# Kernel tuning notes

Hardware: AMD Instinct MI355X
Metric: run time of the kernel (lower is better)

Reference implementation:

```python
import jax, jax.numpy as jnp
import numpy as np

N = 100000   # nodes
E = 1600000  # edges
S = 4        # state_dimension
H = 64       # hidden_channels


def _gcn_conv(x, row, col, W, b):
    """PyG GCNConv: h = x @ W; add self-loops; symmetric deg^-1/2 norm; scatter-add; + bias."""
    n = x.shape[0]
    h = x @ W  # [N, out]
    loop = jnp.arange(n, dtype=row.dtype)
    r = jnp.concatenate([row, loop])  # sources (with self-loops)
    c = jnp.concatenate([col, loop])  # targets (with self-loops)
    deg = jax.ops.segment_sum(jnp.ones(r.shape[0], h.dtype), c, num_segments=n)
    dinv = jnp.where(deg > 0, jax.lax.rsqrt(deg), 0.0)
    norm = dinv[r] * dinv[c]                      # [E+N]
    msg = h[r] * norm[:, None]                    # gather + scale, [E+N, out]
    out = jax.ops.segment_sum(msg, c, num_segments=n)  # scatter-add
    return out + b


def setup_inputs() -> dict:
    key = jax.random.key(0)
    k1, k2, k3, k4 = jax.random.split(key, 4)
    x = jax.random.normal(k1, (N, S), dtype=jnp.float32)
    edge_index = jax.random.randint(k2, (2, E), 0, N, dtype=jnp.int32)
    # Glorot-ish init for the two GCNConv linear layers (+ zero bias, PyG default)
    W1 = jax.random.normal(k3, (S, H), dtype=jnp.float32) * (1.0 / np.sqrt(S))
    b1 = jnp.zeros((H,), jnp.float32)
    W2 = jax.random.normal(k4, (H, S), dtype=jnp.float32) * (1.0 / np.sqrt(H))
    b2 = jnp.zeros((S,), jnp.float32)
    return {"x": x, "edge_index": edge_index, "W1": W1, "b1": b1, "W2": W2, "b2": b2}


def reference(x, edge_index, W1, b1, W2, b2):
    row, col = edge_index[0], edge_index[1]
    h = _gcn_conv(x, row, col, W1, b1)
    h = jax.nn.relu(h)
    out = _gcn_conv(h, row, col, W2, b2)
    return out
```

## Files before the change

kernel.cpp:

```cpp
#include <hip/hip_runtime.h>


#define CSHIFT 10
#define CNODES 1024
#define KC_MAX 128
#define CAPC   18432
#define EPB    4096
#define CURPAD 16
#define HCAP   9216
#define ANODES 128
#define ACAP   2432

__global__ void k_zero(int* __restrict__ p, int n) {
    int i = blockIdx.x * blockDim.x + threadIdx.x;
    if (i < n) p[i] = 0;
}

__global__ void __launch_bounds__(512) k_part(
        const int* __restrict__ row, const int* __restrict__ col,
        int e, int Kc, int* __restrict__ cursor, unsigned* __restrict__ ere) {
    __shared__ int h[KC_MAX];
    __shared__ int loff[KC_MAX];
    __shared__ int gbase[KC_MAX];
    __shared__ int lcur[KC_MAX];
    __shared__ unsigned staged[EPB];
    int t = threadIdx.x;
    if (t < KC_MAX) h[t] = 0;
    __syncthreads();
    int lo = blockIdx.x * EPB;
    int cbuf[8], rbuf[8];
#pragma unroll
    for (int k = 0; k < 8; ++k) {
        int i = lo + t + k * 512;
        if (i < e) { cbuf[k] = col[i]; rbuf[k] = row[i]; }
        else { cbuf[k] = -1; rbuf[k] = 0; }
    }
#pragma unroll
    for (int k = 0; k < 8; ++k)
        if (cbuf[k] >= 0) atomicAdd(&h[cbuf[k] >> CSHIFT], 1);
    __syncthreads();
    if (t < KC_MAX) loff[t] = h[t];
    __syncthreads();
    for (int off = 1; off < KC_MAX; off <<= 1) {
        int v = (t < KC_MAX && t >= off) ? loff[t - off] : 0;
        __syncthreads();
        if (t < KC_MAX) loff[t] += v;
        __syncthreads();
    }
    if (t < KC_MAX) {
        int st = loff[t] - h[t];
        loff[t] = st;
        lcur[t] = st;
        if (t < Kc && h[t]) gbase[t] = atomicAdd(&cursor[t * CURPAD], h[t]);
    }
    __syncthreads();
#pragma unroll
    for (int k = 0; k < 8; ++k) {
        int c = cbuf[k];
        if (c < 0) continue;
        int pos = atomicAdd(&lcur[c >> CSHIFT], 1);
        staged[pos] = ((unsigned)rbuf[k] << CSHIFT) | (unsigned)(c & (CNODES - 1));
    }
    __syncthreads();
    int wid = t >> 6, lane = t & 63;
    for (int k = wid; k < Kc; k += 8) {
        int len = h[k];
        if (!len) continue;
        int gb = gbase[k], lb = loff[k];
        size_t dst = (size_t)k * CAPC + gb;
        for (int j = lane; j < len; j += 64)
            if (gb + j < CAPC) ere[dst + j] = staged[lb + j];
    }
}

__global__ void __launch_bounds__(1024) k_sortH(
        const int* __restrict__ cursor, unsigned* __restrict__ ere,
        int* __restrict__ rstart, const float4* __restrict__ x,
        float* __restrict__ dinv, float4* __restrict__ y, int n) {
    __shared__ int hist[CNODES];
    __shared__ int scn[CNODES];
    __shared__ unsigned sorted[HCAP];
    int b = blockIdx.x >> 1, half = blockIdx.x & 1;
    int t = threadIdx.x, nlo = b << CSHIFT;
    hist[t] = 0;
    __syncthreads();
    size_t c0 = (size_t)b * CAPC;
    int m = min(cursor[b * CURPAD], CAPC);
    int n4 = m >> 2;
    const uint4* e4 = (const uint4*)(ere + c0);
    for (int g = t; g < n4; g += 1024) {
        uint4 w = e4[g];
        atomicAdd(&hist[w.x & (CNODES - 1)], 1);
        atomicAdd(&hist[w.y & (CNODES - 1)], 1);
        atomicAdd(&hist[w.z & (CNODES - 1)], 1);
        atomicAdd(&hist[w.w & (CNODES - 1)], 1);
    }
    for (int i = (n4 << 2) + t; i < m; i += 1024)
        atomicAdd(&hist[ere[c0 + i] & (CNODES - 1)], 1);
    __syncthreads();
    int hv = hist[t];
    scn[t] = hv;
    __syncthreads();
    for (int off = 1; off < CNODES; off <<= 1) {
        int v = (t >= off) ? scn[t - off] : 0;
        __syncthreads();
        scn[t] += v;
        __syncthreads();
    }
    int st = scn[t] - hv;
    int hb1 = scn[511];
    rstart[(b << CSHIFT) + t] = (int)c0 + st;
    if ((t >> 9) == half) {
        int node = nlo + t;
        if (node < n) {
            float di = rsqrtf((float)hv + 1.0f);
            dinv[node] = di;
            float4 xv = x[node];
            y[node] = make_float4(xv.x * di, xv.y * di, xv.z * di, xv.w * di);
        }
    }
    int base = half ? hb1 : 0;
    int cnt = half ? (m - hb1) : hb1;
    __syncthreads();
    scn[t] = st - base;
    __syncthreads();
    for (int g = t; g < n4; g += 1024) {
        uint4 w = e4[g];
        int l0 = w.x & (CNODES - 1);
        if ((l0 >> 9) == half) { int p = atomicAdd(&scn[l0], 1); if (p < HCAP) sorted[p] = w.x >> CSHIFT; }
        int l1 = w.y & (CNODES - 1);
        if ((l1 >> 9) == half) { int p = atomicAdd(&scn[l1], 1); if (p < HCAP) sorted[p] = w.y >> CSHIFT; }
        int l2 = w.z & (CNODES - 1);
        if ((l2 >> 9) == half) { int p = atomicAdd(&scn[l2], 1); if (p < HCAP) sorted[p] = w.z >> CSHIFT; }
        int l3 = w.w & (CNODES - 1);
        if ((l3 >> 9) == half) { int p = atomicAdd(&scn[l3], 1); if (p < HCAP) sorted[p] = w.w >> CSHIFT; }
    }
    for (int i = (n4 << 2) + t; i < m; i += 1024) {
        unsigned w = ere[c0 + i];
        int ln = w & (CNODES - 1);
        if ((ln >> 9) == half) { int p = atomicAdd(&scn[ln], 1); if (p < HCAP) sorted[p] = w >> CSHIFT; }
    }
    __syncthreads();
    int wb = min(cnt, HCAP);
    for (int i = t; i < wb; i += 1024) ere[c0 + base + i] = sorted[i];
}

__global__ void __launch_bounds__(512) k_mid(
        const unsigned* __restrict__ ere, const int* __restrict__ rstart,
        const int* __restrict__ cursor, const float* __restrict__ dinv,
        const float4* __restrict__ x, const float4* __restrict__ y,
        const float* __restrict__ W1, const float* __restrict__ b1,
        const float* __restrict__ W2, const float* __restrict__ b2,
        float4* __restrict__ z, float4* __restrict__ out, int n) {
    __shared__ unsigned recs[ACAP];
    __shared__ float4 sums[ANODES];
    int g = blockIdx.x, t = threadIdx.x;
    int nlo = g * ANODES;
    int b = nlo >> CSHIFT;
    int c0i = (int)((size_t)b * CAPC);
    int s0 = rstart[nlo];
    int e0 = ((g & 7) == 7) ? c0i + min(cursor[b * CURPAD], CAPC)
                            : rstart[nlo + ANODES];
    int len = min(e0 - s0, ACAP);
    for (int i = t; i < len; i += 512) recs[i] = ere[s0 + i];
    __syncthreads();
    int tt = t >> 2, q = t & 3;
    int s = rstart[nlo + tt] - s0;
    int epos = (tt == ANODES - 1) ? len : min(rstart[nlo + tt + 1] - s0, len);
    float vx = 0.f, vy = 0.f, vz = 0.f, vw = 0.f;
    int i = s + q;
    while (i + 12 < epos) {
        int r0 = recs[i], r1 = recs[i + 4], r2 = recs[i + 8], r3 = recs[i + 12];
        float4 a0 = y[r0], a1 = y[r1], a2 = y[r2], a3 = y[r3];
        vx += a0.x + a1.x + a2.x + a3.x;
        vy += a0.y + a1.y + a2.y + a3.y;
        vz += a0.z + a1.z + a2.z + a3.z;
        vw += a0.w + a1.w + a2.w + a3.w;
        i += 16;
    }
    for (; i < epos; i += 4) {
        float4 a = y[recs[i]];
        vx += a.x; vy += a.y; vz += a.z; vw += a.w;
    }
    vx += __shfl_xor(vx, 1); vx += __shfl_xor(vx, 2);
    vy += __shfl_xor(vy, 1); vy += __shfl_xor(vy, 2);
    vz += __shfl_xor(vz, 1); vz += __shfl_xor(vz, 2);
    vw += __shfl_xor(vw, 1); vw += __shfl_xor(vw, 2);
    if (q == 0) sums[tt] = make_float4(vx, vy, vz, vw);
    __syncthreads();
    int node = nlo + t;
    if (t < ANODES && node < n) {
        float di = dinv[node], sl = di * di;
        float4 sv = sums[t];
        float4 xv = x[node];
        float a0 = di * sv.x + xv.x * sl;
        float a1 = di * sv.y + xv.y * sl;
        float a2 = di * sv.z + xv.z * sl;
        float a3 = di * sv.w + xv.w * sl;
        float t0 = 0.f, t1 = 0.f, t2 = 0.f, t3 = 0.f;
#pragma unroll 8
        for (int j = 0; j < 64; ++j) {
            float h = b1[j] + a0 * W1[j] + a1 * W1[64 + j] + a2 * W1[128 + j] + a3 * W1[192 + j];
            h = fmaxf(h, 0.f);
            t0 += h * W2[j * 4 + 0];
            t1 += h * W2[j * 4 + 1];
            t2 += h * W2[j * 4 + 2];
            t3 += h * W2[j * 4 + 3];
        }
        z[node] = make_float4(t0 * di, t1 * di, t2 * di, t3 * di);
        out[node] = make_float4(b2[0] + t0 * sl, b2[1] + t1 * sl,
                                b2[2] + t2 * sl, b2[3] + t3 * sl);
    }
}

__global__ void __launch_bounds__(512) k_acc2(
        const unsigned* __restrict__ ere, const int* __restrict__ rstart,
        const int* __restrict__ cursor, const float* __restrict__ dinv,
        const float4* __restrict__ z, float4* __restrict__ out, int n) {
    __shared__ unsigned recs[ACAP];
    __shared__ float4 sums[ANODES];
    int g = blockIdx.x, t = threadIdx.x;
    int nlo = g * ANODES;
    int b = nlo >> CSHIFT;
    int c0i = (int)((size_t)b * CAPC);
    int s0 = rstart[nlo];
    int e0 = ((g & 7) == 7) ? c0i + min(cursor[b * CURPAD], CAPC)
                            : rstart[nlo + ANODES];
    int len = min(e0 - s0, ACAP);
    for (int i = t; i < len; i += 512) recs[i] = ere[s0 + i];
    __syncthreads();
    int tt = t >> 2, q = t & 3;
    int s = rstart[nlo + tt] - s0;
    int epos = (tt == ANODES - 1) ? len : min(rstart[nlo + tt + 1] - s0, len);
    float vx = 0.f, vy = 0.f, vz = 0.f, vw = 0.f;
    int i = s + q;
    while (i + 12 < epos) {
        int r0 = recs[i], r1 = recs[i + 4], r2 = recs[i + 8], r3 = recs[i + 12];
        float4 a0 = z[r0], a1 = z[r1], a2 = z[r2], a3 = z[r3];
        vx += a0.x + a1.x + a2.x + a3.x;
        vy += a0.y + a1.y + a2.y + a3.y;
        vz += a0.z + a1.z + a2.z + a3.z;
        vw += a0.w + a1.w + a2.w + a3.w;
        i += 16;
    }
    for (; i < epos; i += 4) {
        float4 a = z[recs[i]];
        vx += a.x; vy += a.y; vz += a.z; vw += a.w;
    }
    vx += __shfl_xor(vx, 1); vx += __shfl_xor(vx, 2);
    vy += __shfl_xor(vy, 1); vy += __shfl_xor(vy, 2);
    vz += __shfl_xor(vz, 1); vz += __shfl_xor(vz, 2);
    vw += __shfl_xor(vw, 1); vw += __shfl_xor(vw, 2);
    if (q == 0) sums[tt] = make_float4(vx, vy, vz, vw);
    __syncthreads();
    int node = nlo + t;
    if (t < ANODES && node < n) {
        float di = dinv[node];
        float4 sv = sums[t];
        float4 o = out[node];
        out[node] = make_float4(o.x + di * sv.x, o.y + di * sv.y,
                                o.z + di * sv.z, o.w + di * sv.w);
    }
}

extern "C" void kernel_launch(void* const* d_in, const int* in_sizes, int n_in,
                              void* d_out, int out_size, void* d_ws, size_t ws_size,
                              hipStream_t stream) {
    const float* x  = (const float*)d_in[0];
    const int* edge = (const int*)d_in[1];
    const float* W1 = (const float*)d_in[2];
    const float* b1 = (const float*)d_in[3];
    const float* W2 = (const float*)d_in[4];
    const float* b2 = (const float*)d_in[5];
    float* out = (float*)d_out;

    const int n = in_sizes[0] / 4;
    const int e = in_sizes[1] / 2;
    const int* row = edge;
    const int* col = edge + e;
    const int Kc = (n + CNODES - 1) >> CSHIFT;

    char* ws = (char*)d_ws;
    float* y    = (float*)ws;  ws += (size_t)4 * n * 4;
    float* zmid = (float*)ws;  ws += (size_t)4 * n * 4;
    float* dinv = (float*)ws;  ws += (size_t)n * 4;
    unsigned* ere = (unsigned*)ws;  ws += (size_t)Kc * CAPC * 4;
    int* cursor = (int*)ws;    ws += (size_t)Kc * CURPAD * 4;
    int* rstart = (int*)ws;    ws += (size_t)Kc * CNODES * 4;

    const int B = 256;
    const int gp = (e + EPB - 1) / EPB;
    const int ga = (n + ANODES - 1) / ANODES;
    const int nz = Kc * CURPAD;

    k_zero<<<(nz + B - 1) / B, B, 0, stream>>>(cursor, nz);
    k_part<<<gp, 512, 0, stream>>>(row, col, e, Kc, cursor, ere);
    k_sortH<<<2 * Kc, 1024, 0, stream>>>(cursor, ere, rstart, (const float4*)x,
                                         dinv, (float4*)y, n);
    k_mid<<<ga, 512, 0, stream>>>(ere, rstart, cursor, dinv, (const float4*)x,
                                  (const float4*)y, W1, b1, W2, b2,
                                  (float4*)zmid, (float4*)out, n);
    k_acc2<<<ga, 512, 0, stream>>>(ere, rstart, cursor, dinv,
                                   (const float4*)zmid, (float4*)out, n);
}
```

Before: 125.9 us.

## Fuse sort, layer-1 aggregation, MLP and layer-2 aggregation into one persistent kernel

Merges k_sortH, k_mid and k_acc2 into a single kernel of 2*Kc blocks (about 196). Two software grid barriers replace the kernel boundaries. Each half-cluster block keeps its sorted source list in shared memory and reuses it for both aggregation passes, so the sorted edges are no longer written back to global memory and dinv/rstart arrays are dropped. This removes two launches and the global round trips, but relies on all blocks being co-resident for the spin barrier. Each block also now handles 512 nodes with only 2 threads per node for the gathers, which lowers parallelism.

```diff
diff --git a/kernel.cpp b/kernel.cpp
--- a/kernel.cpp
+++ b/kernel.cpp
@@ -8,8 +8,6 @@
 #define EPB    4096
 #define CURPAD 16
 #define HCAP   9216
-#define ANODES 128
-#define ACAP   2432
 
 __global__ void k_zero(int* __restrict__ p, int n) {
     int i = blockIdx.x * blockDim.x + threadIdx.x;
@@ -73,16 +71,37 @@
     }
 }
 
-__global__ void __launch_bounds__(1024) k_sortH(
-        const int* __restrict__ cursor, unsigned* __restrict__ ere,
-        int* __restrict__ rstart, const float4* __restrict__ x,
-        float* __restrict__ dinv, float4* __restrict__ y, int n) {
-    __shared__ int hist[CNODES];
-    __shared__ int scn[CNODES];
+__device__ __forceinline__ void grid_barrier(int* bar, int nb, int t) {
+    __syncthreads();
+    if (t == 0) {
+        __threadfence();
+        atomicAdd(bar, 1);
+        while (atomicAdd(bar, 0) < nb) { }
+        __threadfence();
+    }
+    __syncthreads();
+}
+
+__global__ void __launch_bounds__(1024) k_mega(
+        const int* __restrict__ cursor, const unsigned* __restrict__ ere,
+        const float4* __restrict__ x,
+        const float* __restrict__ W1, const float* __restrict__ b1,
+        const float* __restrict__ W2, const float* __restrict__ b2,
+        float4* __restrict__ y, float4* __restrict__ z,
+        float4* __restrict__ out, int n, int nb, int* __restrict__ bar) {
+    __shared__ int hist[512];
+    __shared__ int scn[512];
+    __shared__ int cur[512];
+    __shared__ float4 sums[512];
     __shared__ unsigned sorted[HCAP];
-    int b = blockIdx.x >> 1, half = blockIdx.x & 1;
-    int t = threadIdx.x, nlo = b << CSHIFT;
-    hist[t] = 0;
+
+    int bh = blockIdx.x;
+    int b = bh >> 1, h = bh & 1;
+    int t = threadIdx.x;
+    int nlo = (b << CSHIFT) + (h << 9);
+    int node = nlo + t;
+
+    if (t < 512) hist[t] = 0;
     __syncthreads();
     size_t c0 = (size_t)b * CAPC;
     int m = min(cursor[b * CURPAD], CAPC);
@@ -90,176 +109,132 @@
     const uint4* e4 = (const uint4*)(ere + c0);
     for (int g = t; g < n4; g += 1024) {
         uint4 w = e4[g];
-        atomicAdd(&hist[w.x & (CNODES - 1)], 1);
-        atomicAdd(&hist[w.y & (CNODES - 1)], 1);
-        atomicAdd(&hist[w.z & (CNODES - 1)], 1);
-        atomicAdd(&hist[w.w & (CNODES - 1)], 1);
-    }
-    for (int i = (n4 << 2) + t; i < m; i += 1024)
-        atomicAdd(&hist[ere[c0 + i] & (CNODES - 1)], 1);
-    __syncthreads();
-    int hv = hist[t];
-    scn[t] = hv;
-    __syncthreads();
-    for (int off = 1; off < CNODES; off <<= 1) {
-        int v = (t >= off) ? scn[t - off] : 0;
-        __syncthreads();
-        scn[t] += v;
-        __syncthreads();
-    }
-    int st = scn[t] - hv;
-    int hb1 = scn[511];
-    rstart[(b << CSHIFT) + t] = (int)c0 + st;
-    if ((t >> 9) == half) {
-        int node = nlo + t;
+        int l0 = w.x & (CNODES - 1); if ((l0 >> 9) == h) atomicAdd(&hist[l0 & 511], 1);
+        int l1 = w.y & (CNODES - 1); if ((l1 >> 9) == h) atomicAdd(&hist[l1 & 511], 1);
+        int l2 = w.z & (CNODES - 1); if ((l2 >> 9) == h) atomicAdd(&hist[l2 & 511], 1);
+        int l3 = w.w & (CNODES - 1); if ((l3 >> 9) == h) atomicAdd(&hist[l3 & 511], 1);
+    }
+    for (int i = (n4 << 2) + t; i < m; i += 1024) {
+        int l = ere[c0 + i] & (CNODES - 1);
+        if ((l >> 9) == h) atomicAdd(&hist[l & 511], 1);
+    }
+    __syncthreads();
+    int hv = (t < 512) ? hist[t] : 0;
+    if (t < 512) scn[t] = hv;
+    __syncthreads();
+    for (int off = 1; off < 512; off <<= 1) {
+        int v = (t < 512 && t >= off) ? scn[t - off] : 0;
+        __syncthreads();
+        if (t < 512) scn[t] += v;
+        __syncthreads();
+    }
+    float di = 0.f;
+    float4 xv = make_float4(0.f, 0.f, 0.f, 0.f);
+    if (t < 512) {
+        int st = scn[t] - hv;
+        scn[t] = st;
+        cur[t] = st;
         if (node < n) {
-            float di = rsqrtf((float)hv + 1.0f);
-            dinv[node] = di;
-            float4 xv = x[node];
+            di = rsqrtf((float)hv + 1.0f);
+            xv = x[node];
             y[node] = make_float4(xv.x * di, xv.y * di, xv.z * di, xv.w * di);
         }
     }
-    int base = half ? hb1 : 0;
-    int cnt = half ? (m - hb1) : hb1;
-    __syncthreads();
-    scn[t] = st - base;
-    __syncthreads();
+    grid_barrier(bar + 0, nb, t);
+
     for (int g = t; g < n4; g += 1024) {
         uint4 w = e4[g];
         int l0 = w.x & (CNODES - 1);
-        if ((l0 >> 9) == half) { int p = atomicAdd(&scn[l0], 1); if (p < HCAP) sorted[p] = w.x >> CSHIFT; }
+        if ((l0 >> 9) == h) { int p = atomicAdd(&cur[l0 & 511], 1); if (p < HCAP) sorted[p] = w.x >> CSHIFT; }
         int l1 = w.y & (CNODES - 1);
-        if ((l1 >> 9) == half) { int p = atomicAdd(&scn[l1], 1); if (p < HCAP) sorted[p] = w.y >> CSHIFT; }
+        if ((l1 >> 9) == h) { int p = atomicAdd(&cur[l1 & 511], 1); if (p < HCAP) sorted[p] = w.y >> CSHIFT; }
         int l2 = w.z & (CNODES - 1);
-        if ((l2 >> 9) == half) { int p = atomicAdd(&scn[l2], 1); if (p < HCAP) sorted[p] = w.z >> CSHIFT; }
+        if ((l2 >> 9) == h) { int p = atomicAdd(&cur[l2 & 511], 1); if (p < HCAP) sorted[p] = w.z >> CSHIFT; }
         int l3 = w.w & (CNODES - 1);
-        if ((l3 >> 9) == half) { int p = atomicAdd(&scn[l3], 1); if (p < HCAP) sorted[p] = w.w >> CSHIFT; }
+        if ((l3 >> 9) == h) { int p = atomicAdd(&cur[l3 & 511], 1); if (p < HCAP) sorted[p] = w.w >> CSHIFT; }
     }
     for (int i = (n4 << 2) + t; i < m; i += 1024) {
         unsigned w = ere[c0 + i];
-        int ln = w & (CNODES - 1);
-        if ((ln >> 9) == half) { int p = atomicAdd(&scn[ln], 1); if (p < HCAP) sorted[p] = w >> CSHIFT; }
-    }
-    __syncthreads();
-    int wb = min(cnt, HCAP);
-    for (int i = t; i < wb; i += 1024) ere[c0 + base + i] = sorted[i];
-}
-
-__global__ void __launch_bounds__(512) k_mid(
-        const unsigned* __restrict__ ere, const int* __restrict__ rstart,
-        const int* __restrict__ cursor, const float* __restrict__ dinv,
-        const float4* __restrict__ x, const float4* __restrict__ y,
-        const float* __restrict__ W1, const float* __restrict__ b1,
-        const float* __restrict__ W2, const float* __restrict__ b2,
-        float4* __restrict__ z, float4* __restrict__ out, int n) {
-    __shared__ unsigned recs[ACAP];
-    __shared__ float4 sums[ANODES];
-    int g = blockIdx.x, t = threadIdx.x;
-    int nlo = g * ANODES;
-    int b = nlo >> CSHIFT;
-    int c0i = (int)((size_t)b * CAPC);
-    int s0 = rstart[nlo];
-    int e0 = ((g & 7) == 7) ? c0i + min(cursor[b * CURPAD], CAPC)
-                            : rstart[nlo + ANODES];
-    int len = min(e0 - s0, ACAP);
-    for (int i = t; i < len; i += 512) recs[i] = ere[s0 + i];
-    __syncthreads();
-    int tt = t >> 2, q = t & 3;
-    int s = rstart[nlo + tt] - s0;
-    int epos = (tt == ANODES - 1) ? len : min(rstart[nlo + tt + 1] - s0, len);
-    float vx = 0.f, vy = 0.f, vz = 0.f, vw = 0.f;
-    int i = s + q;
-    while (i + 12 < epos) {
-        int r0 = recs[i], r1 = recs[i + 4], r2 = recs[i + 8], r3 = recs[i + 12];
-        float4 a0 = y[r0], a1 = y[r1], a2 = y[r2], a3 = y[r3];
-        vx += a0.x + a1.x + a2.x + a3.x;
-        vy += a0.y + a1.y + a2.y + a3.y;
-        vz += a0.z + a1.z + a2.z + a3.z;
-        vw += a0.w + a1.w + a2.w + a3.w;
-        i += 16;
-    }
-    for (; i < epos; i += 4) {
-        float4 a = y[recs[i]];
-        vx += a.x; vy += a.y; vz += a.z; vw += a.w;
-    }
-    vx += __shfl_xor(vx, 1); vx += __shfl_xor(vx, 2);
-    vy += __shfl_xor(vy, 1); vy += __shfl_xor(vy, 2);
-    vz += __shfl_xor(vz, 1); vz += __shfl_xor(vz, 2);
-    vw += __shfl_xor(vw, 1); vw += __shfl_xor(vw, 2);
-    if (q == 0) sums[tt] = make_float4(vx, vy, vz, vw);
-    __syncthreads();
-    int node = nlo + t;
-    if (t < ANODES && node < n) {
-        float di = dinv[node], sl = di * di;
+        int l = w & (CNODES - 1);
+        if ((l >> 9) == h) { int p = atomicAdd(&cur[l & 511], 1); if (p < HCAP) sorted[p] = w >> CSHIFT; }
+    }
+    __syncthreads();
+    int tt = t >> 1, q = t & 1;
+    int s = scn[tt];
+    int ep = min(s + hist[tt], HCAP);
+    {
+        float vx = 0.f, vy = 0.f, vz = 0.f, vw = 0.f;
+        int i = s + q;
+        while (i + 6 < ep) {
+            unsigned r0 = sorted[i], r1 = sorted[i + 2], r2 = sorted[i + 4], r3 = sorted[i + 6];
+            float4 a0 = y[r0], a1 = y[r1], a2 = y[r2], a3 = y[r3];
+            vx += a0.x + a1.x + a2.x + a3.x;
+            vy += a0.y + a1.y + a2.y + a3.y;
+            vz += a0.z + a1.z + a2.z + a3.z;
+            vw += a0.w + a1.w + a2.w + a3.w;
+            i += 8;
+        }
+        for (; i < ep; i += 2) {
+            float4 a = y[sorted[i]];
+            vx += a.x; vy += a.y; vz += a.z; vw += a.w;
+        }
+        vx += __shfl_xor(vx, 1);
+        vy += __shfl_xor(vy, 1);
+        vz += __shfl_xor(vz, 1);
+        vw += __shfl_xor(vw, 1);
+        if (q == 0) sums[tt] = make_float4(vx, vy, vz, vw);
+    }
+    __syncthreads();
+    float t0 = 0.f, t1 = 0.f, t2 = 0.f, t3 = 0.f;
+    float sl = di * di;
+    if (t < 512 && node < n) {
         float4 sv = sums[t];
-        float4 xv = x[node];
         float a0 = di * sv.x + xv.x * sl;
         float a1 = di * sv.y + xv.y * sl;
         float a2 = di * sv.z + xv.z * sl;
         float a3 = di * sv.w + xv.w * sl;
-        float t0 = 0.f, t1 = 0.f, t2 = 0.f, t3 = 0.f;
 #pragma unroll 8
         for (int j = 0; j < 64; ++j) {
-            float h = b1[j] + a0 * W1[j] + a1 * W1[64 + j] + a2 * W1[128 + j] + a3 * W1[192 + j];
-            h = fmaxf(h, 0.f);
-            t0 += h * W2[j * 4 + 0];
-            t1 += h * W2[j * 4 + 1];
-            t2 += h * W2[j * 4 + 2];
-            t3 += h * W2[j * 4 + 3];
+            float hh = b1[j] + a0 * W1[j] + a1 * W1[64 + j] + a2 * W1[128 + j] + a3 * W1[192 + j];
+            hh = fmaxf(hh, 0.f);
+            t0 += hh * W2[j * 4 + 0];
+            t1 += hh * W2[j * 4 + 1];
+            t2 += hh * W2[j * 4 + 2];
+            t3 += hh * W2[j * 4 + 3];
         }
         z[node] = make_float4(t0 * di, t1 * di, t2 * di, t3 * di);
-        out[node] = make_float4(b2[0] + t0 * sl, b2[1] + t1 * sl,
-                                b2[2] + t2 * sl, b2[3] + t3 * sl);
-    }
-}
-
-__global__ void __launch_bounds__(512) k_acc2(
-        const unsigned* __restrict__ ere, const int* __restrict__ rstart,
-        const int* __restrict__ cursor, const float* __restrict__ dinv,
-        const float4* __restrict__ z, float4* __restrict__ out, int n) {
-    __shared__ unsigned recs[ACAP];
-    __shared__ float4 sums[ANODES];
-    int g = blockIdx.x, t = threadIdx.x;
-    int nlo = g * ANODES;
-    int b = nlo >> CSHIFT;
-    int c0i = (int)((size_t)b * CAPC);
-    int s0 = rstart[nlo];
-    int e0 = ((g & 7) == 7) ? c0i + min(cursor[b * CURPAD], CAPC)
-                            : rstart[nlo + ANODES];
-    int len = min(e0 - s0, ACAP);
-    for (int i = t; i < len; i += 512) recs[i] = ere[s0 + i];
-    __syncthreads();
-    int tt = t >> 2, q = t & 3;
-    int s = rstart[nlo + tt] - s0;
-    int epos = (tt == ANODES - 1) ? len : min(rstart[nlo + tt + 1] - s0, len);
-    float vx = 0.f, vy = 0.f, vz = 0.f, vw = 0.f;
-    int i = s + q;
-    while (i + 12 < epos) {
-        int r0 = recs[i], r1 = recs[i + 4], r2 = recs[i + 8], r3 = recs[i + 12];
-        float4 a0 = z[r0], a1 = z[r1], a2 = z[r2], a3 = z[r3];
-        vx += a0.x + a1.x + a2.x + a3.x;
-        vy += a0.y + a1.y + a2.y + a3.y;
-        vz += a0.z + a1.z + a2.z + a3.z;
-        vw += a0.w + a1.w + a2.w + a3.w;
-        i += 16;
-    }
-    for (; i < epos; i += 4) {
-        float4 a = z[recs[i]];
-        vx += a.x; vy += a.y; vz += a.z; vw += a.w;
-    }
-    vx += __shfl_xor(vx, 1); vx += __shfl_xor(vx, 2);
-    vy += __shfl_xor(vy, 1); vy += __shfl_xor(vy, 2);
-    vz += __shfl_xor(vz, 1); vz += __shfl_xor(vz, 2);
-    vw += __shfl_xor(vw, 1); vw += __shfl_xor(vw, 2);
-    if (q == 0) sums[tt] = make_float4(vx, vy, vz, vw);
-    __syncthreads();
-    int node = nlo + t;
-    if (t < ANODES && node < n) {
-        float di = dinv[node];
+    }
+    grid_barrier(bar + 1, nb, t);
+
+    {
+        float vx = 0.f, vy = 0.f, vz = 0.f, vw = 0.f;
+        int i = s + q;
+        while (i + 6 < ep) {
+            unsigned r0 = sorted[i], r1 = sorted[i + 2], r2 = sorted[i + 4], r3 = sorted[i + 6];
+            float4 a0 = z[r0], a1 = z[r1], a2 = z[r2], a3 = z[r3];
+            vx += a0.x + a1.x + a2.x + a3.x;
+            vy += a0.y + a1.y + a2.y + a3.y;
+            vz += a0.z + a1.z + a2.z + a3.z;
+            vw += a0.w + a1.w + a2.w + a3.w;
+            i += 8;
+        }
+        for (; i < ep; i += 2) {
+            float4 a = z[sorted[i]];
+            vx += a.x; vy += a.y; vz += a.z; vw += a.w;
+        }
+        vx += __shfl_xor(vx, 1);
+        vy += __shfl_xor(vy, 1);
+        vz += __shfl_xor(vz, 1);
+        vw += __shfl_xor(vw, 1);
+        if (q == 0) sums[tt] = make_float4(vx, vy, vz, vw);
+    }
+    __syncthreads();
+    if (t < 512 && node < n) {
         float4 sv = sums[t];
-        float4 o = out[node];
-        out[node] = make_float4(o.x + di * sv.x, o.y + di * sv.y,
-                                o.z + di * sv.z, o.w + di * sv.w);
+        out[node] = make_float4(b2[0] + t0 * sl + di * sv.x,
+                                b2[1] + t1 * sl + di * sv.y,
+                                b2[2] + t2 * sl + di * sv.z,
+                                b2[3] + t3 * sl + di * sv.w);
     }
 }
 
@@ -279,27 +254,23 @@
     const int* row = edge;
     const int* col = edge + e;
     const int Kc = (n + CNODES - 1) >> CSHIFT;
+    const int nb = 2 * Kc;
 
     char* ws = (char*)d_ws;
     float* y    = (float*)ws;  ws += (size_t)4 * n * 4;
     float* zmid = (float*)ws;  ws += (size_t)4 * n * 4;
-    float* dinv = (float*)ws;  ws += (size_t)n * 4;
     unsigned* ere = (unsigned*)ws;  ws += (size_t)Kc * CAPC * 4;
     int* cursor = (int*)ws;    ws += (size_t)Kc * CURPAD * 4;
-    int* rstart = (int*)ws;    ws += (size_t)Kc * CNODES * 4;
+    int* bar    = (int*)ws;    ws += 8 * 4;
 
     const int B = 256;
     const int gp = (e + EPB - 1) / EPB;
-    const int ga = (n + ANODES - 1) / ANODES;
-    const int nz = Kc * CURPAD;
+    const int nz = Kc * CURPAD + 8;
 
     k_zero<<<(nz + B - 1) / B, B, 0, stream>>>(cursor, nz);
     k_part<<<gp, 512, 0, stream>>>(row, col, e, Kc, cursor, ere);
-    k_sortH<<<2 * Kc, 1024, 0, stream>>>(cursor, ere, rstart, (const float4*)x,
-                                         dinv, (float4*)y, n);
-    k_mid<<<ga, 512, 0, stream>>>(ere, rstart, cursor, dinv, (const float4*)x,
-                                  (const float4*)y, W1, b1, W2, b2,
-                                  (float4*)zmid, (float4*)out, n);
-    k_acc2<<<ga, 512, 0, stream>>>(ere, rstart, cursor, dinv,
-                                   (const float4*)zmid, (float4*)out, n);
-}
+    k_mega<<<nb, 1024, 0, stream>>>(cursor, ere, (const float4*)x,
+                                    W1, b1, W2, b2,
+                                    (float4*)y, (float4*)zmid,
+                                    (float4*)out, n, nb, bar);
+}
```

After: 147.9 us. 1.18x slower.
